# Kernel optimization log

Hardware: AMD Instinct MI355X
Metric: run time of the kernel (lower is better)

Reference implementation:

```python
import jax, jax.numpy as jnp
import numpy as np

N_USER, N_MOVIE, H, E = 100000, 50000, 512, 500000

def setup_inputs() -> dict:
    key = jax.random.key(0)
    ks = jax.random.split(key, 8)
    z_user = jax.random.normal(ks[0], (N_USER, H), dtype=jnp.float32)
    z_movie = jax.random.normal(ks[1], (N_MOVIE, H), dtype=jnp.float32)
    edge_row = jax.random.randint(ks[2], (E,), 0, N_USER, dtype=jnp.int64)
    edge_col = jax.random.randint(ks[3], (E,), 0, N_MOVIE, dtype=jnp.int64)
    w1 = jax.random.normal(ks[4], (2 * H, H), dtype=jnp.float32) * (1.0 / np.sqrt(2 * H))
    b1 = jax.random.normal(ks[5], (H,), dtype=jnp.float32) * 0.01
    w2 = jax.random.normal(ks[6], (H, 1), dtype=jnp.float32) * (1.0 / np.sqrt(H))
    b2 = jax.random.normal(ks[7], (1,), dtype=jnp.float32) * 0.01
    return {"z_user": z_user, "z_movie": z_movie, "edge_row": edge_row,
            "edge_col": edge_col, "w1": w1, "b1": b1, "w2": w2, "b2": b2}

def reference(z_user, z_movie, edge_row, edge_col, w1, b1, w2, b2):
    # Gather endpoint embeddings and concat -> [E, 2H]
    z = jnp.concatenate([z_user[edge_row], z_movie[edge_col]], axis=-1)
    h = jax.nn.relu(z @ w1 + b1)      # [E, H]
    out = h @ w2 + b2                 # [E, 1]
    return out.reshape(-1)
```

## Files before the change

kernel.cpp:

```cpp
#include <hip/hip_runtime.h>
#include <hip/hip_bf16.h>

typedef __attribute__((ext_vector_type(8))) short bf16x8;
typedef __attribute__((ext_vector_type(4))) float f32x4;

#define HDIM 512
#define BM 128
#define BN 256
#define BK 64
#define BKP 72

__device__ __forceinline__ unsigned short f2bf(float f) {
  unsigned u = __float_as_uint(f);
  u += 0x7fffu + ((u >> 16) & 1u);
  return (unsigned short)(u >> 16);
}

__device__ __forceinline__ unsigned int pk_bf(float x, float y) {
  __hip_bfloat162 h = __float22bfloat162_rn(float2{x, y});
  union { __hip_bfloat162 b; unsigned int u; } cv; cv.b = h;
  return cv.u;
}

__global__ void k_w1t(const float* __restrict__ w1, unsigned short* __restrict__ w1t) {
  int idx = blockIdx.x * 256 + threadIdx.x;
  int k = idx >> 9;
  int n = idx & 511;
  w1t[n * 1024 + k] = f2bf(w1[idx]);
}

__global__ __launch_bounds__(512) void k_gemm(const float* __restrict__ A, int M,
    const unsigned short* __restrict__ w1t, int koff,
    unsigned short* __restrict__ C)
{
  __shared__ unsigned short As[BM][BKP];
  __shared__ unsigned short Bs[BN][BKP];
  const int tid  = threadIdx.x;
  const int lane = tid & 63;
  const int wid  = tid >> 6;
  const int wm = wid & 1, wn = wid >> 1;
  const int lm = lane & 15, lq = lane >> 4;
  const int nbase = blockIdx.x * BN;
  const int mbase = blockIdx.y * BM;

  f32x4 acc[4][4];
  #pragma unroll
  for (int i = 0; i < 4; ++i)
    #pragma unroll
    for (int j = 0; j < 4; ++j) acc[i][j] = (f32x4){0.f, 0.f, 0.f, 0.f};

  for (int kb = 0; kb < HDIM / BK; ++kb) {
    const int k0 = kb * BK;
    __syncthreads();
    #pragma unroll
    for (int i = 0; i < 4; ++i) {
      int fid = i * 512 + tid;
      int r = fid >> 4, c4 = fid & 15;
      int row = mbase + r; if (row > M - 1) row = M - 1;
      const float4 v = *(const float4*)&A[(size_t)row * HDIM + k0 + c4 * 4];
      unsigned int* dst = (unsigned int*)&As[r][c4 * 4];
      dst[0] = pk_bf(v.x, v.y);
      dst[1] = pk_bf(v.z, v.w);
    }
    #pragma unroll
    for (int i = 0; i < 4; ++i) {
      int cid = i * 512 + tid;
      int r = cid >> 3, c8 = cid & 7;
      const bf16x8 g = *(const bf16x8*)&w1t[(size_t)(nbase + r) * 1024 + koff + k0 + c8 * 8];
      *(bf16x8*)&Bs[r][c8 * 8] = g;
    }
    __syncthreads();
    #pragma unroll
    for (int ks = 0; ks < 2; ++ks) {
      bf16x8 af[4], bfr[4];
      #pragma unroll
      for (int t = 0; t < 4; ++t) {
        af[t]  = *(const bf16x8*)&As[wm * 64 + t * 16 + lm][ks * 32 + lq * 8];
        bfr[t] = *(const bf16x8*)&Bs[wn * 64 + t * 16 + lm][ks * 32 + lq * 8];
      }
      #pragma unroll
      for (int mi = 0; mi < 4; ++mi)
        #pragma unroll
        for (int ni = 0; ni < 4; ++ni)
          acc[mi][ni] = __builtin_amdgcn_mfma_f32_16x16x32_bf16(af[mi], bfr[ni], acc[mi][ni], 0, 0, 0);
    }
  }
  #pragma unroll
  for (int mi = 0; mi < 4; ++mi)
    #pragma unroll
    for (int ni = 0; ni < 4; ++ni)
      #pragma unroll
      for (int r = 0; r < 4; ++r) {
        int rg = mbase + wm * 64 + mi * 16 + lq * 4 + r;
        int cg = nbase + wn * 64 + ni * 16 + lm;
        if (rg < M) C[(size_t)rg * HDIM + cg] = f2bf(acc[mi][ni][r]);
      }
}

__global__ __launch_bounds__(256) void k_edge(const int* __restrict__ er, const int* __restrict__ ec,
    const unsigned short* __restrict__ u1, const unsigned short* __restrict__ m1,
    const float* __restrict__ b1, const float* __restrict__ w2, const float* __restrict__ b2,
    float* __restrict__ out, int E)
{
  const int lane = threadIdx.x & 63;
  const int gwid = blockIdx.x * 4 + (threadIdx.x >> 6);
  const int nw   = gridDim.x * 4;
  const float4 b1a = *(const float4*)&b1[lane * 8];
  const float4 b1b = *(const float4*)&b1[lane * 8 + 4];
  const float4 w2a = *(const float4*)&w2[lane * 8];
  const float4 w2b = *(const float4*)&w2[lane * 8 + 4];
  const float bias2 = b2[0];
  for (int e = gwid * 2; e < E; e += nw * 2) {
    const int r0 = er[e], c0 = ec[e];
    const int r1 = er[e + 1], c1 = ec[e + 1];
    const uint4 ua0 = *(const uint4*)&u1[(size_t)r0 * HDIM + lane * 8];
    const uint4 va0 = *(const uint4*)&m1[(size_t)c0 * HDIM + lane * 8];
    const uint4 ua1 = *(const uint4*)&u1[(size_t)r1 * HDIM + lane * 8];
    const uint4 va1 = *(const uint4*)&m1[(size_t)c1 * HDIM + lane * 8];
    float p0 = 0.f, p1 = 0.f, s;
    s = __uint_as_float(ua0.x << 16)        + __uint_as_float(va0.x << 16)        + b1a.x; s = fmaxf(s, 0.f); p0 += s * w2a.x;
    s = __uint_as_float(ua0.x & 0xffff0000u)+ __uint_as_float(va0.x & 0xffff0000u)+ b1a.y; s = fmaxf(s, 0.f); p0 += s * w2a.y;
    s = __uint_as_float(ua0.y << 16)        + __uint_as_float(va0.y << 16)        + b1a.z; s = fmaxf(s, 0.f); p0 += s * w2a.z;
    s = __uint_as_float(ua0.y & 0xffff0000u)+ __uint_as_float(va0.y & 0xffff0000u)+ b1a.w; s = fmaxf(s, 0.f); p0 += s * w2a.w;
    s = __uint_as_float(ua0.z << 16)        + __uint_as_float(va0.z << 16)        + b1b.x; s = fmaxf(s, 0.f); p0 += s * w2b.x;
    s = __uint_as_float(ua0.z & 0xffff0000u)+ __uint_as_float(va0.z & 0xffff0000u)+ b1b.y; s = fmaxf(s, 0.f); p0 += s * w2b.y;
    s = __uint_as_float(ua0.w << 16)        + __uint_as_float(va0.w << 16)        + b1b.z; s = fmaxf(s, 0.f); p0 += s * w2b.z;
    s = __uint_as_float(ua0.w & 0xffff0000u)+ __uint_as_float(va0.w & 0xffff0000u)+ b1b.w; s = fmaxf(s, 0.f); p0 += s * w2b.w;
    s = __uint_as_float(ua1.x << 16)        + __uint_as_float(va1.x << 16)        + b1a.x; s = fmaxf(s, 0.f); p1 += s * w2a.x;
    s = __uint_as_float(ua1.x & 0xffff0000u)+ __uint_as_float(va1.x & 0xffff0000u)+ b1a.y; s = fmaxf(s, 0.f); p1 += s * w2a.y;
    s = __uint_as_float(ua1.y << 16)        + __uint_as_float(va1.y << 16)        + b1a.z; s = fmaxf(s, 0.f); p1 += s * w2a.z;
    s = __uint_as_float(ua1.y & 0xffff0000u)+ __uint_as_float(va1.y & 0xffff0000u)+ b1a.w; s = fmaxf(s, 0.f); p1 += s * w2a.w;
    s = __uint_as_float(ua1.z << 16)        + __uint_as_float(va1.z << 16)        + b1b.x; s = fmaxf(s, 0.f); p1 += s * w2b.x;
    s = __uint_as_float(ua1.z & 0xffff0000u)+ __uint_as_float(va1.z & 0xffff0000u)+ b1b.y; s = fmaxf(s, 0.f); p1 += s * w2b.y;
    s = __uint_as_float(ua1.w << 16)        + __uint_as_float(va1.w << 16)        + b1b.z; s = fmaxf(s, 0.f); p1 += s * w2b.z;
    s = __uint_as_float(ua1.w & 0xffff0000u)+ __uint_as_float(va1.w & 0xffff0000u)+ b1b.w; s = fmaxf(s, 0.f); p1 += s * w2b.w;
    #pragma unroll
    for (int off = 32; off > 0; off >>= 1) {
      p0 += __shfl_down(p0, off, 64);
      p1 += __shfl_down(p1, off, 64);
    }
    if (lane == 0) *(float2*)&out[e] = float2{p0 + bias2, p1 + bias2};
  }
}

__global__ __launch_bounds__(256) void k_fallback(const float* __restrict__ zu, const float* __restrict__ zm,
    const int* __restrict__ er, const int* __restrict__ ec, const float* __restrict__ w1,
    const float* __restrict__ b1, const float* __restrict__ w2, const float* __restrict__ b2,
    float* __restrict__ out, int E)
{
  __shared__ float Zs[64][33];
  __shared__ float Ws[32][65];
  __shared__ float outacc[64];
  __shared__ int ridx[64], cidx[64];
  const int tid = threadIdx.x;
  const int ebase = blockIdx.x * 64;
  if (tid < 64) {
    int e = ebase + tid; if (e > E - 1) e = E - 1;
    ridx[tid] = er[e]; cidx[tid] = ec[e];
    outacc[tid] = 0.f;
  }
  const int tx = tid & 15, ty = tid >> 4;
  for (int nt = 0; nt < 8; ++nt) {
    float acc[4][4] = {};
    for (int kc = 0; kc < 32; ++kc) {
      __syncthreads();
      #pragma unroll
      for (int i = 0; i < 8; ++i) {
        int id = i * 256 + tid;
        int rr = id >> 5, cc = id & 31;
        int k = kc * 32 + cc;
        Zs[rr][cc] = (k < 512) ? zu[(size_t)ridx[rr] * 512 + k]
                               : zm[(size_t)cidx[rr] * 512 + (k - 512)];
      }
      #pragma unroll
      for (int i = 0; i < 8; ++i) {
        int id = i * 256 + tid;
        int kk = id >> 6, nn = id & 63;
        Ws[kk][nn] = w1[(size_t)(kc * 32 + kk) * 512 + nt * 64 + nn];
      }
      __syncthreads();
      #pragma unroll
      for (int kk = 0; kk < 32; ++kk) {
        float a0 = Zs[ty*4+0][kk], a1 = Zs[ty*4+1][kk], a2 = Zs[ty*4+2][kk], a3 = Zs[ty*4+3][kk];
        float q0 = Ws[kk][tx*4+0], q1 = Ws[kk][tx*4+1], q2 = Ws[kk][tx*4+2], q3 = Ws[kk][tx*4+3];
        acc[0][0] += a0*q0; acc[0][1] += a0*q1; acc[0][2] += a0*q2; acc[0][3] += a0*q3;
        acc[1][0] += a1*q0; acc[1][1] += a1*q1; acc[1][2] += a1*q2; acc[1][3] += a1*q3;
        acc[2][0] += a2*q0; acc[2][1] += a2*q1; acc[2][2] += a2*q2; acc[2][3] += a2*q3;
        acc[3][0] += a3*q0; acc[3][1] += a3*q1; acc[3][2] += a3*q2; acc[3][3] += a3*q3;
      }
    }
    #pragma unroll
    for (int i = 0; i < 4; ++i) {
      float p = 0.f;
      #pragma unroll
      for (int j = 0; j < 4; ++j) {
        int n = nt * 64 + tx * 4 + j;
        float h = acc[i][j] + b1[n]; h = fmaxf(h, 0.f);
        p += h * w2[n];
      }
      atomicAdd(&outacc[ty * 4 + i], p);
    }
  }
  __syncthreads();
  if (tid < 64 && (ebase + tid) < E) out[ebase + tid] = outacc[tid] + b2[0];
}

extern "C" void kernel_launch(void* const* d_in, const int* in_sizes, int n_in,
                              void* d_out, int out_size, void* d_ws, size_t ws_size,
                              hipStream_t stream)
{
  const float* z_user  = (const float*)d_in[0];
  const float* z_movie = (const float*)d_in[1];
  const int*   erow    = (const int*)d_in[2];
  const int*   ecol    = (const int*)d_in[3];
  const float* w1      = (const float*)d_in[4];
  const float* b1      = (const float*)d_in[5];
  const float* w2      = (const float*)d_in[6];
  const float* b2      = (const float*)d_in[7];
  float* out = (float*)d_out;

  const int NU = in_sizes[0] / HDIM;
  const int NM = in_sizes[1] / HDIM;
  const int E  = in_sizes[2];

  const size_t need = ((size_t)NU * HDIM + (size_t)NM * HDIM + (size_t)1024 * 512) * 2;
  if (ws_size >= need) {
    unsigned short* u1  = (unsigned short*)d_ws;
    unsigned short* m1  = u1 + (size_t)NU * HDIM;
    unsigned short* w1t = m1 + (size_t)NM * HDIM;
    k_w1t<<<(1024 * 512) / 256, 256, 0, stream>>>(w1, w1t);
    k_gemm<<<dim3(HDIM / BN, (NU + BM - 1) / BM), 512, 0, stream>>>(z_user,  NU, w1t, 0,   u1);
    k_gemm<<<dim3(HDIM / BN, (NM + BM - 1) / BM), 512, 0, stream>>>(z_movie, NM, w1t, 512, m1);
    k_edge<<<2048, 256, 0, stream>>>(erow, ecol, u1, m1, b1, w2, b2, out, E);
  } else {
    k_fallback<<<(E + 63) / 64, 256, 0, stream>>>(z_user, z_movie, erow, ecol, w1, b1, w2, b2, out, E);
  }
}
```

Measured before the change: 592.9 us.

## Merge user/movie GEMMs into one launch with direct-to-LDS swizzled weight loads

The two per-table GEMM launches become a single launch whose blocks pick the user or movie table by block index. Each block now loops over both N tiles, so it covers the full 512 columns while keeping the same A rows. The B tile is loaded with global_load_lds into an XOR-swizzled LDS layout, skipping the register round trip. Address offsets are precomputed and launch bounds ask for 4 blocks per CU. The trade-off is that A (fp32) is reloaded and converted for each N tile, and each block does more serial work, so there are fewer blocks to spread across CUs.

```diff
diff --git a/kernel.cpp b/kernel.cpp
--- a/kernel.cpp
+++ b/kernel.cpp
@@ -29,72 +29,103 @@
   w1t[n * 1024 + k] = f2bf(w1[idx]);
 }
 
-__global__ __launch_bounds__(512) void k_gemm(const float* __restrict__ A, int M,
-    const unsigned short* __restrict__ w1t, int koff,
-    unsigned short* __restrict__ C)
+__global__ __launch_bounds__(512, 4) void k_gemm(
+    const float* __restrict__ zu, int MU,
+    const float* __restrict__ zm, int MM,
+    const unsigned short* __restrict__ w1t,
+    unsigned short* __restrict__ u1, unsigned short* __restrict__ m1,
+    int nMB1)
 {
   __shared__ unsigned short As[BM][BKP];
-  __shared__ unsigned short Bs[BN][BKP];
+  __shared__ unsigned short Bs[BN * BK];
   const int tid  = threadIdx.x;
   const int lane = tid & 63;
   const int wid  = tid >> 6;
   const int wm = wid & 1, wn = wid >> 1;
   const int lm = lane & 15, lq = lane >> 4;
-  const int nbase = blockIdx.x * BN;
-  const int mbase = blockIdx.y * BM;
-
-  f32x4 acc[4][4];
+
+  const float* A; unsigned short* C; int M, koff, mb = blockIdx.x;
+  if (mb < nMB1) { A = zu; C = u1; M = MU; koff = 0; }
+  else           { A = zm; C = m1; M = MM; koff = HDIM; mb -= nMB1; }
+  const int mbase = mb * BM;
+
+  int aoff[4]; unsigned int alds[4];
   #pragma unroll
-  for (int i = 0; i < 4; ++i)
-    #pragma unroll
-    for (int j = 0; j < 4; ++j) acc[i][j] = (f32x4){0.f, 0.f, 0.f, 0.f};
-
-  for (int kb = 0; kb < HDIM / BK; ++kb) {
-    const int k0 = kb * BK;
-    __syncthreads();
-    #pragma unroll
-    for (int i = 0; i < 4; ++i) {
-      int fid = i * 512 + tid;
-      int r = fid >> 4, c4 = fid & 15;
-      int row = mbase + r; if (row > M - 1) row = M - 1;
-      const float4 v = *(const float4*)&A[(size_t)row * HDIM + k0 + c4 * 4];
-      unsigned int* dst = (unsigned int*)&As[r][c4 * 4];
-      dst[0] = pk_bf(v.x, v.y);
-      dst[1] = pk_bf(v.z, v.w);
-    }
-    #pragma unroll
-    for (int i = 0; i < 4; ++i) {
-      int cid = i * 512 + tid;
-      int r = cid >> 3, c8 = cid & 7;
-      const bf16x8 g = *(const bf16x8*)&w1t[(size_t)(nbase + r) * 1024 + koff + k0 + c8 * 8];
-      *(bf16x8*)&Bs[r][c8 * 8] = g;
-    }
-    __syncthreads();
-    #pragma unroll
-    for (int ks = 0; ks < 2; ++ks) {
-      bf16x8 af[4], bfr[4];
-      #pragma unroll
-      for (int t = 0; t < 4; ++t) {
-        af[t]  = *(const bf16x8*)&As[wm * 64 + t * 16 + lm][ks * 32 + lq * 8];
-        bfr[t] = *(const bf16x8*)&Bs[wn * 64 + t * 16 + lm][ks * 32 + lq * 8];
-      }
-      #pragma unroll
-      for (int mi = 0; mi < 4; ++mi)
+  for (int i = 0; i < 4; ++i) {
+    int fid = i * 512 + tid;
+    int r = fid >> 4, c4 = fid & 15;
+    int row = mbase + r; if (row > M - 1) row = M - 1;
+    aoff[i] = row * HDIM + c4 * 4;
+    alds[i] = r * (BKP >> 1) + c4 * 2;
+  }
+  int boff[4];
+  #pragma unroll
+  for (int i = 0; i < 4; ++i) {
+    int f   = i * 8192 + tid * 16;
+    int row = f >> 7;
+    int cb  = (f & 127) ^ ((row & 7) << 4);
+    boff[i] = row * 1024 + (cb >> 1);
+  }
+  auto BsAS3 = (__attribute__((address_space(3))) char*)&Bs[0];
+  unsigned int* Asw = (unsigned int*)&As[0][0];
+  const char* Bsb = (const char*)&Bs[0];
+  const int swzb = (lm & 7) << 4;
+
+  #pragma unroll 1
+  for (int nb = 0; nb < HDIM / BN; ++nb) {
+    const int nbase = nb * BN;
+    const unsigned short* wsrc = w1t + (size_t)nbase * 1024 + koff;
+    f32x4 acc[4][4];
+    #pragma unroll
+    for (int i = 0; i < 4; ++i)
+      #pragma unroll
+      for (int j = 0; j < 4; ++j) acc[i][j] = (f32x4){0.f, 0.f, 0.f, 0.f};
+
+    #pragma unroll 1
+    for (int kb = 0; kb < HDIM / BK; ++kb) {
+      const int k0 = kb * BK;
+      __syncthreads();
+      #pragma unroll
+      for (int i = 0; i < 4; ++i) {
+        const float4 v = *(const float4*)&A[(size_t)(aoff[i] + k0)];
+        Asw[alds[i]]     = pk_bf(v.x, v.y);
+        Asw[alds[i] + 1] = pk_bf(v.z, v.w);
+      }
+      #pragma unroll
+      for (int i = 0; i < 4; ++i) {
+        __builtin_amdgcn_global_load_lds(
+            (const __attribute__((address_space(1))) unsigned int*)(wsrc + boff[i] + k0),
+            (__attribute__((address_space(3))) unsigned int*)(BsAS3 + i * 8192 + wid * 1024),
+            16, 0, 0);
+      }
+      __syncthreads();
+      #pragma unroll
+      for (int ks = 0; ks < 2; ++ks) {
+        const int cbyte = (ks * 64 + lq * 16) ^ swzb;
+        bf16x8 bfr[4];
         #pragma unroll
-        for (int ni = 0; ni < 4; ++ni)
-          acc[mi][ni] = __builtin_amdgcn_mfma_f32_16x16x32_bf16(af[mi], bfr[ni], acc[mi][ni], 0, 0, 0);
-    }
-  }
-  #pragma unroll
-  for (int mi = 0; mi < 4; ++mi)
-    #pragma unroll
-    for (int ni = 0; ni < 4; ++ni)
-      #pragma unroll
-      for (int r = 0; r < 4; ++r) {
-        int rg = mbase + wm * 64 + mi * 16 + lq * 4 + r;
-        int cg = nbase + wn * 64 + ni * 16 + lm;
-        if (rg < M) C[(size_t)rg * HDIM + cg] = f2bf(acc[mi][ni][r]);
-      }
+        for (int t = 0; t < 4; ++t)
+          bfr[t] = *(const bf16x8*)(Bsb + (wn * 64 + t * 16 + lm) * 128 + cbyte);
+        #pragma unroll
+        for (int mi = 0; mi < 4; ++mi) {
+          const bf16x8 af = *(const bf16x8*)&As[wm * 64 + mi * 16 + lm][ks * 32 + lq * 8];
+          #pragma unroll
+          for (int ni = 0; ni < 4; ++ni)
+            acc[mi][ni] = __builtin_amdgcn_mfma_f32_16x16x32_bf16(af, bfr[ni], acc[mi][ni], 0, 0, 0);
+        }
+      }
+    }
+    #pragma unroll
+    for (int mi = 0; mi < 4; ++mi)
+      #pragma unroll
+      for (int ni = 0; ni < 4; ++ni)
+        #pragma unroll
+        for (int r = 0; r < 4; ++r) {
+          int rg = mbase + wm * 64 + mi * 16 + lq * 4 + r;
+          int cg = nbase + wn * 64 + ni * 16 + lm;
+          if (rg < M) C[(size_t)rg * HDIM + cg] = f2bf(acc[mi][ni][r]);
+        }
+  }
 }
 
 __global__ __launch_bounds__(256) void k_edge(const int* __restrict__ er, const int* __restrict__ ec,
@@ -228,9 +259,10 @@
     unsigned short* u1  = (unsigned short*)d_ws;
     unsigned short* m1  = u1 + (size_t)NU * HDIM;
     unsigned short* w1t = m1 + (size_t)NM * HDIM;
+    const int nMB1 = (NU + BM - 1) / BM;
+    const int nMB2 = (NM + BM - 1) / BM;
     k_w1t<<<(1024 * 512) / 256, 256, 0, stream>>>(w1, w1t);
-    k_gemm<<<dim3(HDIM / BN, (NU + BM - 1) / BM), 512, 0, stream>>>(z_user,  NU, w1t, 0,   u1);
-    k_gemm<<<dim3(HDIM / BN, (NM + BM - 1) / BM), 512, 0, stream>>>(z_movie, NM, w1t, 512, m1);
+    k_gemm<<<nMB1 + nMB2, 512, 0, stream>>>(z_user, NU, z_movie, NM, w1t, u1, m1, nMB1);
     k_edge<<<2048, 256, 0, stream>>>(erow, ecol, u1, m1, b1, w2, b2, out, E);
   } else {
     k_fallback<<<(E + 63) / 64, 256, 0, stream>>>(z_user, z_movie, erow, ecol, w1, b1, w2, b2, out, E);
```

Measured after the change: 651.1 us. 9.8% more time.

## Restructure node GEMM to stream A from registers with swizzled LDS-resident weights

Applied to the files above, without the earlier changes.

The two node-projection GEMMs are merged into one launch. Each block now keeps a 128-column panel of transposed W1 (the full K range) in swizzled LDS, filled by direct global-to-LDS loads, while each wave streams its own 64 rows of fp32 activations straight from global memory into registers. This removes the per-k-tile A staging through LDS and the repeated barriers, and it reduces per-kernel launch overhead. The edge kernel is also widened to four edges per wave to increase memory-level parallelism. In exchange, each 512-row chunk of the activations is re-read by four panel blocks, A loads are now uncoalesced 32-byte fragments, and register pressure is higher with the 4x8 accumulator array.

```diff
diff --git a/kernel.cpp b/kernel.cpp
--- a/kernel.cpp
+++ b/kernel.cpp
@@ -5,10 +5,8 @@
 typedef __attribute__((ext_vector_type(4))) float f32x4;
 
 #define HDIM 512
-#define BM 128
-#define BN 256
-#define BK 64
-#define BKP 72
+#define GBM 512
+#define GBN 128
 
 __device__ __forceinline__ unsigned short f2bf(float f) {
   unsigned u = __float_as_uint(f);
@@ -21,6 +19,9 @@
   union { __hip_bfloat162 b; unsigned int u; } cv; cv.b = h;
   return cv.u;
 }
+
+__device__ __forceinline__ float blo(unsigned int u) { return __uint_as_float(u << 16); }
+__device__ __forceinline__ float bhi(unsigned int u) { return __uint_as_float(u & 0xffff0000u); }
 
 __global__ void k_w1t(const float* __restrict__ w1, unsigned short* __restrict__ w1t) {
   int idx = blockIdx.x * 256 + threadIdx.x;
@@ -29,70 +30,113 @@
   w1t[n * 1024 + k] = f2bf(w1[idx]);
 }
 
-__global__ __launch_bounds__(512) void k_gemm(const float* __restrict__ A, int M,
-    const unsigned short* __restrict__ w1t, int koff,
-    unsigned short* __restrict__ C)
-{
-  __shared__ unsigned short As[BM][BKP];
-  __shared__ unsigned short Bs[BN][BKP];
+__global__ __launch_bounds__(512) void k_gemm(
+    const float* __restrict__ zu, int MU,
+    const float* __restrict__ zm, int MM,
+    const unsigned short* __restrict__ w1t,
+    unsigned short* __restrict__ u1, unsigned short* __restrict__ m1,
+    int nCH1)
+{
+  __shared__ unsigned short Bs[2 * GBN * 256];
   const int tid  = threadIdx.x;
   const int lane = tid & 63;
   const int wid  = tid >> 6;
-  const int wm = wid & 1, wn = wid >> 1;
   const int lm = lane & 15, lq = lane >> 4;
-  const int nbase = blockIdx.x * BN;
-  const int mbase = blockIdx.y * BM;
-
-  f32x4 acc[4][4];
+
+  int chunk = blockIdx.x >> 2, panel = blockIdx.x & 3;
+  const float* A; unsigned short* C; int M, koff, mbase;
+  if (chunk < nCH1) { A = zu; C = u1; M = MU; koff = 0;    mbase = chunk * GBM; }
+  else              { A = zm; C = m1; M = MM; koff = HDIM; mbase = (chunk - nCH1) * GBM; }
+  const int nbase = panel * GBN;
+
+  auto ldsb = (__attribute__((address_space(3))) char*)&Bs[0];
+
+  #pragma unroll
+  for (int i = 0; i < 8; ++i) {
+    int f = i * 8192 + tid * 16;
+    int col = (f >> 9) & 127, cb = f & 511;
+    int kloc = (cb ^ ((col & 7) << 4)) >> 1;
+    const unsigned short* src = w1t + (size_t)(nbase + col) * 1024 + koff + kloc;
+    __builtin_amdgcn_global_load_lds(
+        (const __attribute__((address_space(1))) unsigned int*)src,
+        (__attribute__((address_space(3))) unsigned int*)(ldsb + i * 8192 + wid * 1024),
+        16, 0, 0);
+  }
+  __syncthreads();
+  #pragma unroll
+  for (int i = 8; i < 16; ++i) {
+    int f = i * 8192 + tid * 16;
+    int col = (f >> 9) & 127, cb = f & 511;
+    int kloc = 256 + ((cb ^ ((col & 7) << 4)) >> 1);
+    const unsigned short* src = w1t + (size_t)(nbase + col) * 1024 + koff + kloc;
+    __builtin_amdgcn_global_load_lds(
+        (const __attribute__((address_space(1))) unsigned int*)src,
+        (__attribute__((address_space(3))) unsigned int*)(ldsb + i * 8192 + wid * 1024),
+        16, 0, 0);
+  }
+
+  const float* ap[4];
+  #pragma unroll
+  for (int mi = 0; mi < 4; ++mi) {
+    int row = mbase + wid * 64 + mi * 16 + lm; if (row > M - 1) row = M - 1;
+    ap[mi] = A + (size_t)row * HDIM + lq * 8;
+  }
+
+  f32x4 acc[4][8];
   #pragma unroll
   for (int i = 0; i < 4; ++i)
     #pragma unroll
-    for (int j = 0; j < 4; ++j) acc[i][j] = (f32x4){0.f, 0.f, 0.f, 0.f};
-
-  for (int kb = 0; kb < HDIM / BK; ++kb) {
-    const int k0 = kb * BK;
-    __syncthreads();
-    #pragma unroll
-    for (int i = 0; i < 4; ++i) {
-      int fid = i * 512 + tid;
-      int r = fid >> 4, c4 = fid & 15;
-      int row = mbase + r; if (row > M - 1) row = M - 1;
-      const float4 v = *(const float4*)&A[(size_t)row * HDIM + k0 + c4 * 4];
-      unsigned int* dst = (unsigned int*)&As[r][c4 * 4];
-      dst[0] = pk_bf(v.x, v.y);
-      dst[1] = pk_bf(v.z, v.w);
-    }
-    #pragma unroll
-    for (int i = 0; i < 4; ++i) {
-      int cid = i * 512 + tid;
-      int r = cid >> 3, c8 = cid & 7;
-      const bf16x8 g = *(const bf16x8*)&w1t[(size_t)(nbase + r) * 1024 + koff + k0 + c8 * 8];
-      *(bf16x8*)&Bs[r][c8 * 8] = g;
-    }
-    __syncthreads();
-    #pragma unroll
-    for (int ks = 0; ks < 2; ++ks) {
-      bf16x8 af[4], bfr[4];
-      #pragma unroll
-      for (int t = 0; t < 4; ++t) {
-        af[t]  = *(const bf16x8*)&As[wm * 64 + t * 16 + lm][ks * 32 + lq * 8];
-        bfr[t] = *(const bf16x8*)&Bs[wn * 64 + t * 16 + lm][ks * 32 + lq * 8];
-      }
-      #pragma unroll
-      for (int mi = 0; mi < 4; ++mi)
-        #pragma unroll
-        for (int ni = 0; ni < 4; ++ni)
-          acc[mi][ni] = __builtin_amdgcn_mfma_f32_16x16x32_bf16(af[mi], bfr[ni], acc[mi][ni], 0, 0, 0);
-    }
-  }
+    for (int j = 0; j < 8; ++j) acc[i][j] = (f32x4){0.f, 0.f, 0.f, 0.f};
+
+  const char* bsb = (const char*)&Bs[0];
+  const int swz = (lm & 7) << 4;
+
+  #pragma unroll 4
+  for (int kk = 0; kk < 8; ++kk) {
+    bf16x8 bfr[8];
+    #pragma unroll
+    for (int ni = 0; ni < 8; ++ni)
+      bfr[ni] = *(const bf16x8*)(bsb + (ni * 16 + lm) * 512 + ((kk * 64 + lq * 16) ^ swz));
+    #pragma unroll
+    for (int mi = 0; mi < 4; ++mi) {
+      const float4 v0 = *(const float4*)(ap[mi] + kk * 32);
+      const float4 v1 = *(const float4*)(ap[mi] + kk * 32 + 4);
+      bf16x8 af; unsigned int* aw = (unsigned int*)&af;
+      aw[0] = pk_bf(v0.x, v0.y); aw[1] = pk_bf(v0.z, v0.w);
+      aw[2] = pk_bf(v1.x, v1.y); aw[3] = pk_bf(v1.z, v1.w);
+      #pragma unroll
+      for (int ni = 0; ni < 8; ++ni)
+        acc[mi][ni] = __builtin_amdgcn_mfma_f32_16x16x32_bf16(af, bfr[ni], acc[mi][ni], 0, 0, 0);
+    }
+  }
+  __syncthreads();
+  #pragma unroll 4
+  for (int kk = 8; kk < 16; ++kk) {
+    bf16x8 bfr[8];
+    #pragma unroll
+    for (int ni = 0; ni < 8; ++ni)
+      bfr[ni] = *(const bf16x8*)(bsb + 65536 + (ni * 16 + lm) * 512 + (((kk & 7) * 64 + lq * 16) ^ swz));
+    #pragma unroll
+    for (int mi = 0; mi < 4; ++mi) {
+      const float4 v0 = *(const float4*)(ap[mi] + kk * 32);
+      const float4 v1 = *(const float4*)(ap[mi] + kk * 32 + 4);
+      bf16x8 af; unsigned int* aw = (unsigned int*)&af;
+      aw[0] = pk_bf(v0.x, v0.y); aw[1] = pk_bf(v0.z, v0.w);
+      aw[2] = pk_bf(v1.x, v1.y); aw[3] = pk_bf(v1.z, v1.w);
+      #pragma unroll
+      for (int ni = 0; ni < 8; ++ni)
+        acc[mi][ni] = __builtin_amdgcn_mfma_f32_16x16x32_bf16(af, bfr[ni], acc[mi][ni], 0, 0, 0);
+    }
+  }
+
   #pragma unroll
   for (int mi = 0; mi < 4; ++mi)
     #pragma unroll
-    for (int ni = 0; ni < 4; ++ni)
+    for (int ni = 0; ni < 8; ++ni)
       #pragma unroll
       for (int r = 0; r < 4; ++r) {
-        int rg = mbase + wm * 64 + mi * 16 + lq * 4 + r;
-        int cg = nbase + wn * 64 + ni * 16 + lm;
+        int rg = mbase + wid * 64 + mi * 16 + lq * 4 + r;
+        int cg = nbase + ni * 16 + lm;
         if (rg < M) C[(size_t)rg * HDIM + cg] = f2bf(acc[mi][ni][r]);
       }
 }
@@ -110,36 +154,52 @@
   const float4 w2a = *(const float4*)&w2[lane * 8];
   const float4 w2b = *(const float4*)&w2[lane * 8 + 4];
   const float bias2 = b2[0];
-  for (int e = gwid * 2; e < E; e += nw * 2) {
-    const int r0 = er[e], c0 = ec[e];
-    const int r1 = er[e + 1], c1 = ec[e + 1];
-    const uint4 ua0 = *(const uint4*)&u1[(size_t)r0 * HDIM + lane * 8];
-    const uint4 va0 = *(const uint4*)&m1[(size_t)c0 * HDIM + lane * 8];
-    const uint4 ua1 = *(const uint4*)&u1[(size_t)r1 * HDIM + lane * 8];
-    const uint4 va1 = *(const uint4*)&m1[(size_t)c1 * HDIM + lane * 8];
-    float p0 = 0.f, p1 = 0.f, s;
-    s = __uint_as_float(ua0.x << 16)        + __uint_as_float(va0.x << 16)        + b1a.x; s = fmaxf(s, 0.f); p0 += s * w2a.x;
-    s = __uint_as_float(ua0.x & 0xffff0000u)+ __uint_as_float(va0.x & 0xffff0000u)+ b1a.y; s = fmaxf(s, 0.f); p0 += s * w2a.y;
-    s = __uint_as_float(ua0.y << 16)        + __uint_as_float(va0.y << 16)        + b1a.z; s = fmaxf(s, 0.f); p0 += s * w2a.z;
-    s = __uint_as_float(ua0.y & 0xffff0000u)+ __uint_as_float(va0.y & 0xffff0000u)+ b1a.w; s = fmaxf(s, 0.f); p0 += s * w2a.w;
-    s = __uint_as_float(ua0.z << 16)        + __uint_as_float(va0.z << 16)        + b1b.x; s = fmaxf(s, 0.f); p0 += s * w2b.x;
-    s = __uint_as_float(ua0.z & 0xffff0000u)+ __uint_as_float(va0.z & 0xffff0000u)+ b1b.y; s = fmaxf(s, 0.f); p0 += s * w2b.y;
-    s = __uint_as_float(ua0.w << 16)        + __uint_as_float(va0.w << 16)        + b1b.z; s = fmaxf(s, 0.f); p0 += s * w2b.z;
-    s = __uint_as_float(ua0.w & 0xffff0000u)+ __uint_as_float(va0.w & 0xffff0000u)+ b1b.w; s = fmaxf(s, 0.f); p0 += s * w2b.w;
-    s = __uint_as_float(ua1.x << 16)        + __uint_as_float(va1.x << 16)        + b1a.x; s = fmaxf(s, 0.f); p1 += s * w2a.x;
-    s = __uint_as_float(ua1.x & 0xffff0000u)+ __uint_as_float(va1.x & 0xffff0000u)+ b1a.y; s = fmaxf(s, 0.f); p1 += s * w2a.y;
-    s = __uint_as_float(ua1.y << 16)        + __uint_as_float(va1.y << 16)        + b1a.z; s = fmaxf(s, 0.f); p1 += s * w2a.z;
-    s = __uint_as_float(ua1.y & 0xffff0000u)+ __uint_as_float(va1.y & 0xffff0000u)+ b1a.w; s = fmaxf(s, 0.f); p1 += s * w2a.w;
-    s = __uint_as_float(ua1.z << 16)        + __uint_as_float(va1.z << 16)        + b1b.x; s = fmaxf(s, 0.f); p1 += s * w2b.x;
-    s = __uint_as_float(ua1.z & 0xffff0000u)+ __uint_as_float(va1.z & 0xffff0000u)+ b1b.y; s = fmaxf(s, 0.f); p1 += s * w2b.y;
-    s = __uint_as_float(ua1.w << 16)        + __uint_as_float(va1.w << 16)        + b1b.z; s = fmaxf(s, 0.f); p1 += s * w2b.z;
-    s = __uint_as_float(ua1.w & 0xffff0000u)+ __uint_as_float(va1.w & 0xffff0000u)+ b1b.w; s = fmaxf(s, 0.f); p1 += s * w2b.w;
-    #pragma unroll
-    for (int off = 32; off > 0; off >>= 1) {
-      p0 += __shfl_down(p0, off, 64);
-      p1 += __shfl_down(p1, off, 64);
-    }
-    if (lane == 0) *(float2*)&out[e] = float2{p0 + bias2, p1 + bias2};
+  for (int e = gwid * 4; e < E; e += nw * 4) {
+    if (e + 3 < E) {
+      uint4 ua[4], va[4];
+      #pragma unroll
+      for (int j = 0; j < 4; ++j) {
+        ua[j] = *(const uint4*)&u1[(size_t)er[e + j] * HDIM + lane * 8];
+        va[j] = *(const uint4*)&m1[(size_t)ec[e + j] * HDIM + lane * 8];
+      }
+      float p[4];
+      #pragma unroll
+      for (int j = 0; j < 4; ++j) {
+        float pj = 0.f, s;
+        s = blo(ua[j].x) + blo(va[j].x) + b1a.x; s = fmaxf(s, 0.f); pj += s * w2a.x;
+        s = bhi(ua[j].x) + bhi(va[j].x) + b1a.y; s = fmaxf(s, 0.f); pj += s * w2a.y;
+        s = blo(ua[j].y) + blo(va[j].y) + b1a.z; s = fmaxf(s, 0.f); pj += s * w2a.z;
+        s = bhi(ua[j].y) + bhi(va[j].y) + b1a.w; s = fmaxf(s, 0.f); pj += s * w2a.w;
+        s = blo(ua[j].z) + blo(va[j].z) + b1b.x; s = fmaxf(s, 0.f); pj += s * w2b.x;
+        s = bhi(ua[j].z) + bhi(va[j].z) + b1b.y; s = fmaxf(s, 0.f); pj += s * w2b.y;
+        s = blo(ua[j].w) + blo(va[j].w) + b1b.z; s = fmaxf(s, 0.f); pj += s * w2b.z;
+        s = bhi(ua[j].w) + bhi(va[j].w) + b1b.w; s = fmaxf(s, 0.f); pj += s * w2b.w;
+        p[j] = pj;
+      }
+      #pragma unroll
+      for (int off = 32; off > 0; off >>= 1)
+        #pragma unroll
+        for (int j = 0; j < 4; ++j) p[j] += __shfl_down(p[j], off, 64);
+      if (lane == 0)
+        *(float4*)&out[e] = float4{p[0] + bias2, p[1] + bias2, p[2] + bias2, p[3] + bias2};
+    } else {
+      for (int j = 0; j < 4 && e + j < E; ++j) {
+        const uint4 ua = *(const uint4*)&u1[(size_t)er[e + j] * HDIM + lane * 8];
+        const uint4 va = *(const uint4*)&m1[(size_t)ec[e + j] * HDIM + lane * 8];
+        float pj = 0.f, s;
+        s = blo(ua.x) + blo(va.x) + b1a.x; s = fmaxf(s, 0.f); pj += s * w2a.x;
+        s = bhi(ua.x) + bhi(va.x) + b1a.y; s = fmaxf(s, 0.f); pj += s * w2a.y;
+        s = blo(ua.y) + blo(va.y) + b1a.z; s = fmaxf(s, 0.f); pj += s * w2a.z;
+        s = bhi(ua.y) + bhi(va.y) + b1a.w; s = fmaxf(s, 0.f); pj += s * w2a.w;
+        s = blo(ua.z) + blo(va.z) + b1b.x; s = fmaxf(s, 0.f); pj += s * w2b.x;
+        s = bhi(ua.z) + bhi(va.z) + b1b.y; s = fmaxf(s, 0.f); pj += s * w2b.y;
+        s = blo(ua.w) + blo(va.w) + b1b.z; s = fmaxf(s, 0.f); pj += s * w2b.z;
+        s = bhi(ua.w) + bhi(va.w) + b1b.w; s = fmaxf(s, 0.f); pj += s * w2b.w;
+        #pragma unroll
+        for (int off = 32; off > 0; off >>= 1) pj += __shfl_down(pj, off, 64);
+        if (lane == 0) out[e + j] = pj + bias2;
+      }
+    }
   }
 }
 
@@ -228,9 +288,10 @@
     unsigned short* u1  = (unsigned short*)d_ws;
     unsigned short* m1  = u1 + (size_t)NU * HDIM;
     unsigned short* w1t = m1 + (size_t)NM * HDIM;
+    const int nCH1 = (NU + GBM - 1) / GBM;
+    const int nCH2 = (NM + GBM - 1) / GBM;
     k_w1t<<<(1024 * 512) / 256, 256, 0, stream>>>(w1, w1t);
-    k_gemm<<<dim3(HDIM / BN, (NU + BM - 1) / BM), 512, 0, stream>>>(z_user,  NU, w1t, 0,   u1);
-    k_gemm<<<dim3(HDIM / BN, (NM + BM - 1) / BM), 512, 0, stream>>>(z_movie, NM, w1t, 512, m1);
+    k_gemm<<<(nCH1 + nCH2) * 4, 512, 0, stream>>>(z_user, NU, z_movie, NM, w1t, u1, m1, nCH1);
     k_edge<<<2048, 256, 0, stream>>>(erow, ecol, u1, m1, b1, w2, b2, out, E);
   } else {
     k_fallback<<<(E + 63) / 64, 256, 0, stream>>>(z_user, z_movie, erow, ecol, w1, b1, w2, b2, out, E);
```

Result: slower. 676.9 us (+14.2%).

## Merge user/movie GEMMs into one launch and register-prefetch next K tile

Applied to the files above, without the earlier changes.

The two per-table GEMM launches are merged into a single grid whose y-blocks select either the user or the movie table, removing one launch and its tail. The K loop now loads the next tile's A and B into registers right after the LDS barrier, so the global loads overlap the MFMA work on the current tile. Load offsets and LDS addresses are precomputed once per thread. This holds more live registers, which could lower occupancy under the 512-thread launch bound.

```diff
diff --git a/kernel.cpp b/kernel.cpp
--- a/kernel.cpp
+++ b/kernel.cpp
@@ -29,9 +29,12 @@
   w1t[n * 1024 + k] = f2bf(w1[idx]);
 }
 
-__global__ __launch_bounds__(512) void k_gemm(const float* __restrict__ A, int M,
-    const unsigned short* __restrict__ w1t, int koff,
-    unsigned short* __restrict__ C)
+__global__ __launch_bounds__(512) void k_gemm(
+    const float* __restrict__ zu, int MU,
+    const float* __restrict__ zm, int MM,
+    const unsigned short* __restrict__ w1t,
+    unsigned short* __restrict__ u1, unsigned short* __restrict__ m1,
+    int nMB1)
 {
   __shared__ unsigned short As[BM][BKP];
   __shared__ unsigned short Bs[BN][BKP];
@@ -40,8 +43,31 @@
   const int wid  = tid >> 6;
   const int wm = wid & 1, wn = wid >> 1;
   const int lm = lane & 15, lq = lane >> 4;
+
+  const float* A; unsigned short* C; int M, koff, mb = blockIdx.y;
+  if (mb < nMB1) { A = zu; C = u1; M = MU; koff = 0; }
+  else           { A = zm; C = m1; M = MM; koff = HDIM; mb -= nMB1; }
   const int nbase = blockIdx.x * BN;
-  const int mbase = blockIdx.y * BM;
+  const int mbase = mb * BM;
+
+  int aoff[4]; unsigned int alds[4];
+  #pragma unroll
+  for (int i = 0; i < 4; ++i) {
+    int fid = i * 512 + tid;
+    int r = fid >> 4, c4 = fid & 15;
+    int row = mbase + r; if (row > M - 1) row = M - 1;
+    aoff[i] = row * HDIM + c4 * 4;
+    alds[i] = r * (BKP >> 1) + c4 * 2;
+  }
+  int boff[4]; unsigned short* blds[4];
+  #pragma unroll
+  for (int i = 0; i < 4; ++i) {
+    int cid = i * 512 + tid;
+    int r = cid >> 3, c8 = cid & 7;
+    boff[i] = (nbase + r) * 1024 + koff + c8 * 8;
+    blds[i] = &Bs[r][c8 * 8];
+  }
+  unsigned int* Asw = (unsigned int*)&As[0][0];
 
   f32x4 acc[4][4];
   #pragma unroll
@@ -49,27 +75,29 @@
     #pragma unroll
     for (int j = 0; j < 4; ++j) acc[i][j] = (f32x4){0.f, 0.f, 0.f, 0.f};
 
+  float4 areg[4]; bf16x8 breg[4];
+  #pragma unroll
+  for (int i = 0; i < 4; ++i) areg[i] = *(const float4*)&A[(size_t)aoff[i]];
+  #pragma unroll
+  for (int i = 0; i < 4; ++i) breg[i] = *(const bf16x8*)&w1t[(size_t)boff[i]];
+
   for (int kb = 0; kb < HDIM / BK; ++kb) {
-    const int k0 = kb * BK;
     __syncthreads();
     #pragma unroll
     for (int i = 0; i < 4; ++i) {
-      int fid = i * 512 + tid;
-      int r = fid >> 4, c4 = fid & 15;
-      int row = mbase + r; if (row > M - 1) row = M - 1;
-      const float4 v = *(const float4*)&A[(size_t)row * HDIM + k0 + c4 * 4];
-      unsigned int* dst = (unsigned int*)&As[r][c4 * 4];
-      dst[0] = pk_bf(v.x, v.y);
-      dst[1] = pk_bf(v.z, v.w);
-    }
-    #pragma unroll
-    for (int i = 0; i < 4; ++i) {
-      int cid = i * 512 + tid;
-      int r = cid >> 3, c8 = cid & 7;
-      const bf16x8 g = *(const bf16x8*)&w1t[(size_t)(nbase + r) * 1024 + koff + k0 + c8 * 8];
-      *(bf16x8*)&Bs[r][c8 * 8] = g;
-    }
+      Asw[alds[i]]     = pk_bf(areg[i].x, areg[i].y);
+      Asw[alds[i] + 1] = pk_bf(areg[i].z, areg[i].w);
+    }
+    #pragma unroll
+    for (int i = 0; i < 4; ++i) *(bf16x8*)blds[i] = breg[i];
     __syncthreads();
+    if (kb < HDIM / BK - 1) {
+      const int k1 = (kb + 1) * BK;
+      #pragma unroll
+      for (int i = 0; i < 4; ++i) areg[i] = *(const float4*)&A[(size_t)(aoff[i] + k1)];
+      #pragma unroll
+      for (int i = 0; i < 4; ++i) breg[i] = *(const bf16x8*)&w1t[(size_t)(boff[i] + k1)];
+    }
     #pragma unroll
     for (int ks = 0; ks < 2; ++ks) {
       bf16x8 af[4], bfr[4];
@@ -228,9 +256,10 @@
     unsigned short* u1  = (unsigned short*)d_ws;
     unsigned short* m1  = u1 + (size_t)NU * HDIM;
     unsigned short* w1t = m1 + (size_t)NM * HDIM;
+    const int nMB1 = (NU + BM - 1) / BM;
+    const int nMB2 = (NM + BM - 1) / BM;
     k_w1t<<<(1024 * 512) / 256, 256, 0, stream>>>(w1, w1t);
-    k_gemm<<<dim3(HDIM / BN, (NU + BM - 1) / BM), 512, 0, stream>>>(z_user,  NU, w1t, 0,   u1);
-    k_gemm<<<dim3(HDIM / BN, (NM + BM - 1) / BM), 512, 0, stream>>>(z_movie, NM, w1t, 512, m1);
+    k_gemm<<<dim3(HDIM / BN, nMB1 + nMB2), 512, 0, stream>>>(z_user, NU, z_movie, NM, w1t, u1, m1, nMB1);
     k_edge<<<2048, 256, 0, stream>>>(erow, ecol, u1, m1, b1, w2, b2, out, E);
   } else {
     k_fallback<<<(E + 63) / 64, 256, 0, stream>>>(z_user, z_movie, erow, ecol, w1, b1, w2, b2, out, E);
```

Result: faster. 569.6 us (-3.9%).
